# Optimization experiments

Hardware: AMD Instinct MI355X
Metric: run time of the kernel (lower is better)

Reference implementation:

```python
import jax, jax.numpy as jnp
import numpy as np

TEMPERATURE = 1.0
EPS = 1e-12


def _l2_normalize(x, axis):
    # torch F.normalize: x / max(||x||_2, eps)
    n = jnp.sqrt(jnp.sum(x * x, axis=axis, keepdims=True))
    return x / jnp.maximum(n, EPS)


def setup_inputs() -> dict:
    key = jax.random.key(0)
    k1, k2 = jax.random.split(key)
    B, C, H, W = 2, 128, 128, 256
    K = 20
    features = jax.random.normal(k1, (B, C, H, W), dtype=jnp.float32)
    prototypes = jax.random.normal(k2, (K, C), dtype=jnp.float32)
    distance_scale = jnp.ones((1,), dtype=jnp.float32)
    return {"features": features, "prototypes": prototypes, "distance_scale": distance_scale}


def reference(features, prototypes, distance_scale):
    # features: [B, C, H, W] -> transpose(1,3) -> [B, W, H, C]
    f = jnp.transpose(features, (0, 3, 2, 1))
    # torch F.normalize default dim=1: on [B, W, H, C] this is the W axis (faithful)
    fn = _l2_normalize(f, axis=1)
    # prototypes [K, C], normalized along dim=1 (features)
    pn = _l2_normalize(prototypes, axis=1)
    # exact euclidean cdist (donot_use_mm): broadcasted diff [B, W, H, K, C]
    diff = fn[:, :, :, None, :] - pn[None, None, None, :, :]
    dist = jnp.sqrt(jnp.sum(diff * diff, axis=-1))  # [B, W, H, K]
    dist = jnp.abs(distance_scale) * dist
    # transpose(3,1): [B, K, H, W]
    logits = -jnp.transpose(dist, (0, 3, 2, 1))
    return logits / TEMPERATURE
```

## Files before the change

kernel.cpp:

```cpp
#include <hip/hip_runtime.h>
#include <math.h>

#define B 2
#define C 128
#define H 128
#define W 256
#define K 20
#define HW (H * W)

typedef float f32x4 __attribute__((ext_vector_type(4)));
typedef short bf16x8 __attribute__((ext_vector_type(8)));

__device__ __forceinline__ unsigned f2bf_bits(float x) {
    unsigned u = __float_as_uint(x);
    return (u + 0x7FFFu + ((u >> 16) & 1u)) >> 16;
}
__device__ __forceinline__ float bf_to_f(unsigned bits) {
    return __uint_as_float(bits << 16);
}

__global__ __launch_bounds__(256) void isomax_prep(
    const float* __restrict__ feats, const float* __restrict__ protos,
    float* __restrict__ rn_ws, short* __restrict__ pnf_ws, float* __restrict__ ppsum_ws)
{
    const int tid = threadIdx.x, wave = tid >> 6, lane = tid & 63;
    const int blk = blockIdx.x;

    if (blk < 8192) {
        const int r = blk * 4 + wave;
        const float4 v = ((const float4*)(feats + (size_t)r * W))[lane];
        float ss = fmaf(v.x, v.x, fmaf(v.y, v.y, fmaf(v.z, v.z, v.w * v.w)));
        #pragma unroll
        for (int off = 32; off > 0; off >>= 1) ss += __shfl_xor(ss, off, 64);
        if (lane == 0) {
            const int h  = r & (H - 1);
            const int bc = r >> 7;
            const int c  = bc & (C - 1);
            const int b  = bc >> 7;
            rn_ws[(b * H + h) * C + c] = 1.0f / fmaxf(sqrtf(ss), 1e-12f);
        }
    } else {
        __shared__ float s_rp[32];
        for (int k = wave; k < K; k += 4) {
            const float* p = protos + k * C;
            float a = p[lane], bq = p[lane + 64];
            float ss = fmaf(a, a, bq * bq);
            #pragma unroll
            for (int off = 32; off > 0; off >>= 1) ss += __shfl_xor(ss, off, 64);
            if (lane == 0) s_rp[k] = 1.0f / fmaxf(sqrtf(ss), 1e-12f);
        }
        __syncthreads();
        for (int i = tid; i < 4096; i += 256) {
            const int j  = i & 7;
            const int ln = (i >> 3) & 63;
            const int ch = (i >> 9) & 3;
            const int t  = i >> 11;
            const int c  = ch * 32 + ((ln >> 4) & 3) * 8 + j;
            const int k  = t * 16 + (ln & 15);
            float val = (k < K) ? protos[k * C + c] * s_rp[k] : 0.0f;
            pnf_ws[i] = (short)f2bf_bits(val);
        }
        if (tid < 32) {
            float s = 0.f;
            if (tid < K) {
                const float rp = s_rp[tid];
                for (int c = 0; c < C; ++c) {
                    float pb = bf_to_f(f2bf_bits(protos[tid * C + c] * rp));
                    s = fmaf(pb, pb, s);
                }
            }
            ppsum_ws[tid] = s;
        }
    }
}

__global__ __launch_bounds__(256, 4) void isomax_dist(
    const float* __restrict__ feats, const float* __restrict__ rn_ws,
    const short* __restrict__ pnf_ws, const float* __restrict__ ppsum_ws,
    const float* __restrict__ dscale, float* __restrict__ out)
{
    __shared__ float s_u[C * 68];
    __shared__ float s_S[64];

    const int tid  = threadIdx.x;
    const int wave = tid >> 6, lane = tid & 63;
    const int quad = lane >> 4, l16 = lane & 15;
    const int blk  = blockIdx.x;
    const int wq   = blk & 3;
    const int bh   = blk >> 2;
    const int b    = bh >> 7, h = bh & 127;
    const int w0   = wq * 64;

    bf16x8 bfrag[4][2];
    #pragma unroll
    for (int t = 0; t < 2; ++t)
        #pragma unroll
        for (int ch = 0; ch < 4; ++ch)
            bfrag[ch][t] = ((const bf16x8*)pnf_ws)[(t * 4 + ch) * 64 + lane];
    const float pcol0 = ppsum_ws[l16];
    const float pcol1 = ppsum_ws[16 + l16];
    const float scale = fabsf(dscale[0]);

    {
        const int wl = l16 * 4;
        #pragma unroll
        for (int r = 0; r < 8; ++r) {
            const int c  = wave * 32 + quad + r * 4;
            const float rn = rn_ws[bh * C + c];
            const float4 f4 = *(const float4*)(feats + ((size_t)(b * C + c) * H + h) * W + w0 + wl);
            float4 u4;
            u4.x = f4.x * rn; u4.y = f4.y * rn; u4.z = f4.z * rn; u4.w = f4.w * rn;
            const int swz = ((c >> 3) & 1) << 4;
            *(float4*)&s_u[c * 68 + (wl ^ swz)] = u4;
        }
    }
    __syncthreads();

    f32x4 acc0 = {0.f, 0.f, 0.f, 0.f}, acc1 = {0.f, 0.f, 0.f, 0.f};
    float Sp = 0.f;
    const int wm = wave * 16 + l16;
    const int rswz = (quad & 1) << 4;
    #pragma unroll
    for (int ch = 0; ch < 4; ++ch) {
        float uj[8];
        #pragma unroll
        for (int j = 0; j < 8; ++j)
            uj[j] = s_u[(ch * 32 + quad * 8 + j) * 68 + (wm ^ rswz)];
        bf16x8 af;
        #pragma unroll
        for (int j = 0; j < 8; ++j) {
            Sp = fmaf(uj[j], uj[j], Sp);
            af[j] = (short)f2bf_bits(uj[j]);
        }
        acc0 = __builtin_amdgcn_mfma_f32_16x16x32_bf16(af, bfrag[ch][0], acc0, 0, 0, 0);
        acc1 = __builtin_amdgcn_mfma_f32_16x16x32_bf16(af, bfrag[ch][1], acc1, 0, 0, 0);
    }

    Sp += __shfl_xor(Sp, 16, 64);
    Sp += __shfl_xor(Sp, 32, 64);
    if (lane < 16) s_S[wave * 16 + lane] = Sp;
    __syncthreads();

    const float4 sr4 = *(const float4*)&s_S[wave * 16 + quad * 4];
    const float srv[4] = {sr4.x, sr4.y, sr4.z, sr4.w};

    float* s_o = s_u;
    #pragma unroll
    for (int r = 0; r < 4; ++r) {
        const int wl = wave * 16 + quad * 4 + r;
        float d20 = srv[r] + pcol0 - 2.0f * acc0[r];
        s_o[l16 * 68 + wl] = -scale * sqrtf(fmaxf(d20, 0.f));
        if (l16 < 4) {
            float d21 = srv[r] + pcol1 - 2.0f * acc1[r];
            s_o[(16 + l16) * 68 + wl] = -scale * sqrtf(fmaxf(d21, 0.f));
        }
    }
    __syncthreads();

    for (int i = tid; i < K * 16; i += 256) {
        const int k = i >> 4, g = i & 15;
        const float4 v = *(const float4*)&s_o[k * 68 + g * 4];
        *(float4*)(out + (size_t)(b * K + k) * HW + h * W + w0 + g * 4) = v;
    }
}

extern "C" void kernel_launch(void* const* d_in, const int* in_sizes, int n_in,
                              void* d_out, int out_size, void* d_ws, size_t ws_size,
                              hipStream_t stream) {
    const float* feats  = (const float*)d_in[0];
    const float* protos = (const float*)d_in[1];
    const float* dscale = (const float*)d_in[2];
    float* out = (float*)d_out;

    float* rn_ws    = (float*)d_ws;
    float* ppsum_ws = rn_ws + 32768;
    short* pnf_ws   = (short*)(ppsum_ws + 32);

    isomax_prep<<<8193, 256, 0, stream>>>(feats, protos, rn_ws, pnf_ws, ppsum_ws);
    isomax_dist<<<B * H * 4, 256, 0, stream>>>(feats, rn_ws, pnf_ws, ppsum_ws,
                                               dscale, out);
}
```

Baseline: 91.53 us.

## Split channel reduction across waves and load features directly into MFMA fragments

The distance kernel now handles 32 columns per block instead of 64, which doubles the grid. Each pair of waves splits the 128-channel reduction in half, and the partial MFMA accumulators and squared norms are combined through shared memory. Features are read straight from global memory into bf16 A-fragments with per-lane scalar loads, so the large LDS staging tile is gone. LDS use drops and occupancy rises, but the global reads become 4-byte strided loads coalesced over only 16 lanes, and an extra barrier-based reduction step is added.

```diff
diff --git a/kernel.cpp b/kernel.cpp
--- a/kernel.cpp
+++ b/kernel.cpp
@@ -74,93 +74,106 @@
     }
 }
 
-__global__ __launch_bounds__(256, 4) void isomax_dist(
+#define SO_ST 36
+__global__ __launch_bounds__(256, 8) void isomax_dist(
     const float* __restrict__ feats, const float* __restrict__ rn_ws,
     const short* __restrict__ pnf_ws, const float* __restrict__ ppsum_ws,
     const float* __restrict__ dscale, float* __restrict__ out)
 {
-    __shared__ float s_u[C * 68];
-    __shared__ float s_S[64];
+    __shared__ float s_rn[C];
+    __shared__ float s_pp[32];
+    __shared__ float s_part[2][64][8];
+    __shared__ float s_Sh[2][16];
+    __shared__ float s_S[2 * 16];
+    __shared__ __align__(16) float s_o[K * SO_ST];
 
     const int tid  = threadIdx.x;
     const int wave = tid >> 6, lane = tid & 63;
     const int quad = lane >> 4, l16 = lane & 15;
     const int blk  = blockIdx.x;
-    const int wq   = blk & 3;
-    const int bh   = blk >> 2;
+    const int bh   = blk >> 3;
+    const int oct  = blk & 7;
     const int b    = bh >> 7, h = bh & 127;
-    const int w0   = wq * 64;
+    const int w0   = oct * 32;
+    const int mt   = wave >> 1;
+    const int ch0  = (wave & 1) * 2;
 
-    bf16x8 bfrag[4][2];
+    if (tid < C)  s_rn[tid] = rn_ws[bh * C + tid];
+    if (tid < 32) s_pp[tid] = ppsum_ws[tid];
+    __syncthreads();
+
+    bf16x8 bfr[2][2];
     #pragma unroll
     for (int t = 0; t < 2; ++t)
         #pragma unroll
-        for (int ch = 0; ch < 4; ++ch)
-            bfrag[ch][t] = ((const bf16x8*)pnf_ws)[(t * 4 + ch) * 64 + lane];
-    const float pcol0 = ppsum_ws[l16];
-    const float pcol1 = ppsum_ws[16 + l16];
-    const float scale = fabsf(dscale[0]);
+        for (int c2 = 0; c2 < 2; ++c2)
+            bfr[c2][t] = ((const bf16x8*)pnf_ws)[(t * 4 + ch0 + c2) * 64 + lane];
 
-    {
-        const int wl = l16 * 4;
+    f32x4 acc0 = {0.f, 0.f, 0.f, 0.f}, acc1 = {0.f, 0.f, 0.f, 0.f};
+    float Sp = 0.f;
+    const float* fbase = feats + (size_t)b * C * HW + h * W + w0 + mt * 16 + l16;
+    #pragma unroll
+    for (int c2 = 0; c2 < 2; ++c2) {
+        const int ch = ch0 + c2;
+        bf16x8 af;
         #pragma unroll
-        for (int r = 0; r < 8; ++r) {
-            const int c  = wave * 32 + quad + r * 4;
-            const float rn = rn_ws[bh * C + c];
-            const float4 f4 = *(const float4*)(feats + ((size_t)(b * C + c) * H + h) * W + w0 + wl);
-            float4 u4;
-            u4.x = f4.x * rn; u4.y = f4.y * rn; u4.z = f4.z * rn; u4.w = f4.w * rn;
-            const int swz = ((c >> 3) & 1) << 4;
-            *(float4*)&s_u[c * 68 + (wl ^ swz)] = u4;
+        for (int j = 0; j < 8; ++j) {
+            const int c = ch * 32 + quad * 8 + j;
+            const float uf = fbase[(size_t)c * HW] * s_rn[c];
+            const unsigned bits = f2bf_bits(uf);
+            af[j] = (short)bits;
+            const float ur = bf_to_f(bits);
+            Sp = fmaf(ur, ur, Sp);
+        }
+        acc0 = __builtin_amdgcn_mfma_f32_16x16x32_bf16(af, bfr[c2][0], acc0, 0, 0, 0);
+        acc1 = __builtin_amdgcn_mfma_f32_16x16x32_bf16(af, bfr[c2][1], acc1, 0, 0, 0);
+    }
+
+    Sp += __shfl_xor(Sp, 16, 64);
+    Sp += __shfl_xor(Sp, 32, 64);
+
+    if (wave & 1) {
+        #pragma unroll
+        for (int e = 0; e < 4; ++e) {
+            s_part[mt][lane][e]     = acc0[e];
+            s_part[mt][lane][4 + e] = acc1[e];
+        }
+        if (lane < 16) s_Sh[mt][lane] = Sp;
+    }
+    __syncthreads();
+    if (!(wave & 1)) {
+        #pragma unroll
+        for (int e = 0; e < 4; ++e) {
+            acc0[e] += s_part[mt][lane][e];
+            acc1[e] += s_part[mt][lane][4 + e];
+        }
+        const float Sfull = Sp + s_Sh[mt][l16];
+        if (lane < 16) s_S[mt * 16 + lane] = Sfull;
+    }
+    __syncthreads();
+
+    if (!(wave & 1)) {
+        const float scale = fabsf(dscale[0]);
+        const float pcol0 = s_pp[l16];
+        const float pcol1 = (l16 < 4) ? s_pp[16 + l16] : 0.0f;
+        #pragma unroll
+        for (int r = 0; r < 4; ++r) {
+            const int wl = mt * 16 + quad * 4 + r;
+            const float Sm = s_S[wl];
+            const float d20 = fmaxf(Sm + pcol0 - 2.0f * acc0[r], 0.f);
+            s_o[l16 * SO_ST + wl] = -scale * sqrtf(d20);
+            if (l16 < 4) {
+                const float d21 = fmaxf(Sm + pcol1 - 2.0f * acc1[r], 0.f);
+                s_o[(16 + l16) * SO_ST + wl] = -scale * sqrtf(d21);
+            }
         }
     }
     __syncthreads();
 
-    f32x4 acc0 = {0.f, 0.f, 0.f, 0.f}, acc1 = {0.f, 0.f, 0.f, 0.f};
-    float Sp = 0.f;
-    const int wm = wave * 16 + l16;
-    const int rswz = (quad & 1) << 4;
-    #pragma unroll
-    for (int ch = 0; ch < 4; ++ch) {
-        float uj[8];
-        #pragma unroll
-        for (int j = 0; j < 8; ++j)
-            uj[j] = s_u[(ch * 32 + quad * 8 + j) * 68 + (wm ^ rswz)];
-        bf16x8 af;
-        #pragma unroll
-        for (int j = 0; j < 8; ++j) {
-            Sp = fmaf(uj[j], uj[j], Sp);
-            af[j] = (short)f2bf_bits(uj[j]);
-        }
-        acc0 = __builtin_amdgcn_mfma_f32_16x16x32_bf16(af, bfrag[ch][0], acc0, 0, 0, 0);
-        acc1 = __builtin_amdgcn_mfma_f32_16x16x32_bf16(af, bfrag[ch][1], acc1, 0, 0, 0);
-    }
-
-    Sp += __shfl_xor(Sp, 16, 64);
-    Sp += __shfl_xor(Sp, 32, 64);
-    if (lane < 16) s_S[wave * 16 + lane] = Sp;
-    __syncthreads();
-
-    const float4 sr4 = *(const float4*)&s_S[wave * 16 + quad * 4];
-    const float srv[4] = {sr4.x, sr4.y, sr4.z, sr4.w};
-
-    float* s_o = s_u;
-    #pragma unroll
-    for (int r = 0; r < 4; ++r) {
-        const int wl = wave * 16 + quad * 4 + r;
-        float d20 = srv[r] + pcol0 - 2.0f * acc0[r];
-        s_o[l16 * 68 + wl] = -scale * sqrtf(fmaxf(d20, 0.f));
-        if (l16 < 4) {
-            float d21 = srv[r] + pcol1 - 2.0f * acc1[r];
-            s_o[(16 + l16) * 68 + wl] = -scale * sqrtf(fmaxf(d21, 0.f));
-        }
-    }
-    __syncthreads();
-
-    for (int i = tid; i < K * 16; i += 256) {
-        const int k = i >> 4, g = i & 15;
-        const float4 v = *(const float4*)&s_o[k * 68 + g * 4];
-        *(float4*)(out + (size_t)(b * K + k) * HW + h * W + w0 + g * 4) = v;
+    for (int i = tid; i < K * 8; i += 256) {
+        const int k = i >> 3, g = i & 7;
+        const float4 v = *(const float4*)&s_o[k * SO_ST + g * 4];
+        *(float4*)(out + ((size_t)(b * K + k)) * HW + h * W + w0 + g * 4) = v;
     }
 }
 
@@ -177,6 +190,6 @@
     short* pnf_ws   = (short*)(ppsum_ws + 32);
 
     isomax_prep<<<8193, 256, 0, stream>>>(feats, protos, rn_ws, pnf_ws, ppsum_ws);
-    isomax_dist<<<B * H * 4, 256, 0, stream>>>(feats, rn_ws, pnf_ws, ppsum_ws,
+    isomax_dist<<<B * H * 8, 256, 0, stream>>>(feats, rn_ws, pnf_ws, ppsum_ws,
                                                dscale, out);
 }
```

New measurement: 92.10 us. About the same (+0.6%).

## Load features directly into MFMA fragments and drop LDS staging in distance kernel

Applied to the files above, without the earlier changes.

The distance kernel no longer stages normalized features through a 34KB LDS tile. Each lane now loads its scalar features straight from global memory into bf16 MFMA A-fragments and writes float4 outputs directly from the accumulators, which removes two block-wide barriers and the LDS round-trip. Launch bounds rise to 8 blocks per SM. The row norm is now computed from the bf16-rounded values, which changes numerics slightly. The cost is narrower global loads: 16 consecutive floats per row per quad instead of float4 vectors, and only 16-float-wide output stores.

```diff
diff --git a/kernel.cpp b/kernel.cpp
--- a/kernel.cpp
+++ b/kernel.cpp
@@ -74,93 +74,74 @@
     }
 }
 
-__global__ __launch_bounds__(256, 4) void isomax_dist(
+__global__ __launch_bounds__(256, 8) void isomax_dist(
     const float* __restrict__ feats, const float* __restrict__ rn_ws,
     const short* __restrict__ pnf_ws, const float* __restrict__ ppsum_ws,
     const float* __restrict__ dscale, float* __restrict__ out)
 {
-    __shared__ float s_u[C * 68];
-    __shared__ float s_S[64];
+    __shared__ float s_S[4][16];
 
     const int tid  = threadIdx.x;
     const int wave = tid >> 6, lane = tid & 63;
     const int quad = lane >> 4, l16 = lane & 15;
     const int blk  = blockIdx.x;
-    const int wq   = blk & 3;
     const int bh   = blk >> 2;
+    const int q4   = blk & 3;
     const int b    = bh >> 7, h = bh & 127;
-    const int w0   = wq * 64;
+    const int w0   = q4 * 64 + wave * 16;
 
-    bf16x8 bfrag[4][2];
+    bf16x8 bfr[4][2];
     #pragma unroll
     for (int t = 0; t < 2; ++t)
         #pragma unroll
         for (int ch = 0; ch < 4; ++ch)
-            bfrag[ch][t] = ((const bf16x8*)pnf_ws)[(t * 4 + ch) * 64 + lane];
+            bfr[ch][t] = ((const bf16x8*)pnf_ws)[(t * 4 + ch) * 64 + lane];
+
+    const float scale = fabsf(dscale[0]);
     const float pcol0 = ppsum_ws[l16];
-    const float pcol1 = ppsum_ws[16 + l16];
-    const float scale = fabsf(dscale[0]);
+    const float pcol1 = ppsum_ws[16 + (l16 & 3)];
 
-    {
-        const int wl = l16 * 4;
-        #pragma unroll
-        for (int r = 0; r < 8; ++r) {
-            const int c  = wave * 32 + quad + r * 4;
-            const float rn = rn_ws[bh * C + c];
-            const float4 f4 = *(const float4*)(feats + ((size_t)(b * C + c) * H + h) * W + w0 + wl);
-            float4 u4;
-            u4.x = f4.x * rn; u4.y = f4.y * rn; u4.z = f4.z * rn; u4.w = f4.w * rn;
-            const int swz = ((c >> 3) & 1) << 4;
-            *(float4*)&s_u[c * 68 + (wl ^ swz)] = u4;
-        }
-    }
-    __syncthreads();
-
+    const float* fbase = feats + (size_t)b * C * HW + h * W + w0 + l16;
+    const float* rnb   = rn_ws + bh * C;
     f32x4 acc0 = {0.f, 0.f, 0.f, 0.f}, acc1 = {0.f, 0.f, 0.f, 0.f};
     float Sp = 0.f;
-    const int wm = wave * 16 + l16;
-    const int rswz = (quad & 1) << 4;
     #pragma unroll
     for (int ch = 0; ch < 4; ++ch) {
-        float uj[8];
-        #pragma unroll
-        for (int j = 0; j < 8; ++j)
-            uj[j] = s_u[(ch * 32 + quad * 8 + j) * 68 + (wm ^ rswz)];
         bf16x8 af;
         #pragma unroll
         for (int j = 0; j < 8; ++j) {
-            Sp = fmaf(uj[j], uj[j], Sp);
-            af[j] = (short)f2bf_bits(uj[j]);
+            const int c = ch * 32 + quad * 8 + j;
+            const float uf = fbase[(size_t)c * HW] * rnb[c];
+            const unsigned bits = f2bf_bits(uf);
+            af[j] = (short)bits;
+            const float ur = bf_to_f(bits);
+            Sp = fmaf(ur, ur, Sp);
         }
-        acc0 = __builtin_amdgcn_mfma_f32_16x16x32_bf16(af, bfrag[ch][0], acc0, 0, 0, 0);
-        acc1 = __builtin_amdgcn_mfma_f32_16x16x32_bf16(af, bfrag[ch][1], acc1, 0, 0, 0);
+        acc0 = __builtin_amdgcn_mfma_f32_16x16x32_bf16(af, bfr[ch][0], acc0, 0, 0, 0);
+        acc1 = __builtin_amdgcn_mfma_f32_16x16x32_bf16(af, bfr[ch][1], acc1, 0, 0, 0);
     }
 
     Sp += __shfl_xor(Sp, 16, 64);
     Sp += __shfl_xor(Sp, 32, 64);
-    if (lane < 16) s_S[wave * 16 + lane] = Sp;
-    __syncthreads();
+    if (lane < 16) s_S[wave][lane] = Sp;
+    const float4 Sm4 = *(const float4*)&s_S[wave][quad * 4];
 
-    const float4 sr4 = *(const float4*)&s_S[wave * 16 + quad * 4];
-    const float srv[4] = {sr4.x, sr4.y, sr4.z, sr4.w};
-
-    float* s_o = s_u;
+    float4 o0;
     #pragma unroll
     for (int r = 0; r < 4; ++r) {
-        const int wl = wave * 16 + quad * 4 + r;
-        float d20 = srv[r] + pcol0 - 2.0f * acc0[r];
-        s_o[l16 * 68 + wl] = -scale * sqrtf(fmaxf(d20, 0.f));
-        if (l16 < 4) {
-            float d21 = srv[r] + pcol1 - 2.0f * acc1[r];
-            s_o[(16 + l16) * 68 + wl] = -scale * sqrtf(fmaxf(d21, 0.f));
+        const float d2 = fmaxf((&Sm4.x)[r] + pcol0 - 2.0f * acc0[r], 0.f);
+        (&o0.x)[r] = -scale * sqrtf(d2);
+    }
+    *(float4*)(out + ((size_t)(b * K + l16)) * HW + h * W + w0 + quad * 4) = o0;
+
+    if (l16 < 4) {
+        float4 o1;
+        #pragma unroll
+        for (int r = 0; r < 4; ++r) {
+            const float d2 = fmaxf((&Sm4.x)[r] + pcol1 - 2.0f * acc1[r], 0.f);
+            (&o1.x)[r] = -scale * sqrtf(d2);
         }
-    }
-    __syncthreads();
-
-    for (int i = tid; i < K * 16; i += 256) {
-        const int k = i >> 4, g = i & 15;
-        const float4 v = *(const float4*)&s_o[k * 68 + g * 4];
-        *(float4*)(out + (size_t)(b * K + k) * HW + h * W + w0 + g * 4) = v;
+        *(float4*)(out + ((size_t)(b * K + 16 + l16)) * HW + h * W + w0 + quad * 4) = o1;
     }
 }
 
```

After: 95.97 us. 1.05x slower.
